# Optimization experiments

Hardware: AMD Instinct MI355X
Metric: run time of the kernel (lower is better)

The kernel has to match this reference:

```python
import jax, jax.numpy as jnp
import numpy as np
import math

C_S = 256
NUM_HEADS = 8
HEAD_DIM = 32
TOTAL = NUM_HEADS * HEAD_DIM
B, S, I = 1, 256, 256  # batch, msa sequences (column attn axis), residues
LN_EPS = 1e-5


def setup_inputs() -> dict:
    key = jax.random.key(0)
    ks = jax.random.split(key, 10)
    sc = 1.0 / math.sqrt(C_S)
    return {
        "msa": jax.random.normal(ks[0], (B, S, I, C_S), dtype=jnp.float32),
        "ln_gamma": jnp.ones((C_S,), dtype=jnp.float32),
        "ln_beta": jnp.zeros((C_S,), dtype=jnp.float32),
        "Wq": jax.random.normal(ks[1], (C_S, TOTAL), dtype=jnp.float32) * sc,
        "Wk": jax.random.normal(ks[2], (C_S, TOTAL), dtype=jnp.float32) * sc,
        "Wv": jax.random.normal(ks[3], (C_S, TOTAL), dtype=jnp.float32) * sc,
        "Wg": jax.random.normal(ks[4], (C_S, TOTAL), dtype=jnp.float32) * sc,
        "bg": jnp.zeros((TOTAL,), dtype=jnp.float32),
        "Wo": jax.random.normal(ks[5], (TOTAL, C_S), dtype=jnp.float32) * (1.0 / math.sqrt(TOTAL)),
        "bo": jnp.zeros((C_S,), dtype=jnp.float32),
    }


def reference(msa, ln_gamma, ln_beta, Wq, Wk, Wv, Wg, bg, Wo, bo):
    # LayerNorm over channel dim
    mu = jnp.mean(msa, axis=-1, keepdims=True)
    var = jnp.mean(jnp.square(msa - mu), axis=-1, keepdims=True)
    x = (msa - mu) * jax.lax.rsqrt(var + LN_EPS) * ln_gamma + ln_beta

    b, s, i, _ = x.shape
    hd = (NUM_HEADS, HEAD_DIM)
    Q = (x @ Wq).reshape(b, s, i, *hd)
    K = (x @ Wk).reshape(b, s, i, *hd)
    V = (x @ Wv).reshape(b, s, i, *hd)
    G = jax.nn.sigmoid((x @ Wg + bg).reshape(b, s, i, *hd))

    # column attention: contract over head_dim, attend over sequence axis s/t
    scores = jnp.einsum('bsihd,btihd->bihst', Q, K) / math.sqrt(HEAD_DIM)
    attn = jax.nn.softmax(scores, axis=-1)
    vals = jnp.einsum('bihst,btihd->bsihd', attn, V)

    vals = (G * vals).reshape(b, s, i, TOTAL)
    return vals @ Wo + bo
```

## Files before the change

kernel.cpp:

```cpp
#include <hip/hip_runtime.h>
#include <hip/hip_fp16.h>
#include <math.h>

#define C_S 256
#define NUM_HEADS 8
#define HEAD_DIM 32
#define TOTAL 256
#define S_DIM 256
#define I_DIM 256
#define NROWS (S_DIM * I_DIM)
#define LN_EPS 1e-5f

typedef _Float16 f16x8 __attribute__((ext_vector_type(8)));
typedef __attribute__((ext_vector_type(4))) float f32x4;

__device__ __forceinline__ ushort f2h(float x) {
  return __half_as_ushort(__float2half(x));
}
__device__ __forceinline__ float h2f(ushort u) {
  return __half2float(__ushort_as_half(u));
}
__device__ __forceinline__ void gl16(const void* g, void* l) {
  __builtin_amdgcn_global_load_lds(
      (const __attribute__((address_space(1))) unsigned*)g,
      (__attribute__((address_space(3))) unsigned*)l, 16, 0, 0);
}

__global__ __launch_bounds__(256) void prep_w_kernel(
    const float* __restrict__ Wq, const float* __restrict__ Wk,
    const float* __restrict__ Wv, const float* __restrict__ Wg,
    const float* __restrict__ Wo,
    ushort* __restrict__ Wch, ushort* __restrict__ Woh) {
  const int b = blockIdx.x;
  const int mat = b >> 8, n = b & 255;
  const int k = threadIdx.x;
  const float* W = (mat == 0) ? Wq : (mat == 1) ? Wk
                  : (mat == 2) ? Wv : (mat == 3) ? Wg : Wo;
  ushort h = f2h(W[(size_t)k * 256 + n]);
  if (mat < 4) Wch[((size_t)(mat * 256 + n)) * 256 + k] = h;
  else         Woh[(size_t)n * 256 + k] = h;
}

__global__ __launch_bounds__(256) void prep_x_kernel(
    const float* __restrict__ msa, const float* __restrict__ gamma,
    const float* __restrict__ beta, ushort* __restrict__ Xh) {
  const int row  = blockIdx.x * 4 + (threadIdx.x >> 6);
  const int lane = threadIdx.x & 63;
  float4 v = ((const float4*)(msa + (size_t)row * C_S))[lane];
  float sum = v.x + v.y + v.z + v.w;
  float sq  = v.x*v.x + v.y*v.y + v.z*v.z + v.w*v.w;
  #pragma unroll
  for (int off = 1; off < 64; off <<= 1) {
    sum += __shfl_xor(sum, off);
    sq  += __shfl_xor(sq, off);
  }
  float mu = sum * (1.0f / 256.0f);
  float rs = rsqrtf(sq * (1.0f / 256.0f) - mu * mu + LN_EPS);
  float4 gv = ((const float4*)gamma)[lane];
  float4 bv = ((const float4*)beta)[lane];
  ushort4 hh;
  hh.x = f2h((v.x - mu) * rs * gv.x + bv.x);
  hh.y = f2h((v.y - mu) * rs * gv.y + bv.y);
  hh.z = f2h((v.z - mu) * rs * gv.z + bv.z);
  hh.w = f2h((v.w - mu) * rs * gv.w + bv.w);
  *(ushort4*)(Xh + (size_t)row * 256 + lane * 4) = hh;
}

__global__ __launch_bounds__(256) void proj_kernel(
    const ushort* __restrict__ Xh, const ushort* __restrict__ Wch,
    const float* __restrict__ bg,
    ushort* __restrict__ Qh, ushort* __restrict__ Kh,
    ushort* __restrict__ Vh, __half* __restrict__ Gh) {
  __shared__ __align__(16) ushort At0[128 * 32];
  __shared__ __align__(16) ushort At1[128 * 32];
  __shared__ __align__(16) ushort Bt0[128 * 32];
  __shared__ __align__(16) ushort Bt1[128 * 32];

  const int bid = blockIdx.x;
  const int xcd = bid & 7;
  const int j   = bid >> 3;
  const int ntile = j & 7;
  const int rt    = (xcd << 6) + (j >> 3);
  const int n0 = ntile * 128;
  const int r0 = rt * 128;
  const int tid = threadIdx.x;
  const int wave = tid >> 6, lane = tid & 63;
  const int wm = wave >> 1, wn = wave & 1;
  const int lr = lane & 15, quad = lane >> 4;
  const int fsw = (quad ^ ((lr >> 1) & 3)) * 8;

  const int slot = wave * 64 + lane;
  const int row0 = slot >> 2;
  const int kc   = ((slot & 3) ^ ((row0 >> 1) & 3)) * 8;

  const ushort* pA = Xh + (size_t)(r0 + row0) * 256 + kc;
  const ushort* pB = Wch + (size_t)(n0 + row0) * 256 + kc;
  const int ld0 = wave * 512;
  const int ld1 = 2048 + wave * 512;

  f32x4 acc[4][4] = {};

  for (int kk = 0; kk < 4; ++kk) {
    __syncthreads();
    gl16(pA,             At0 + ld0); gl16(pA + 64 * 256,      At0 + ld1);
    gl16(pA + 32,        At1 + ld0); gl16(pA + 64 * 256 + 32, At1 + ld1);
    gl16(pB,             Bt0 + ld0); gl16(pB + 64 * 256,      Bt0 + ld1);
    gl16(pB + 32,        Bt1 + ld0); gl16(pB + 64 * 256 + 32, Bt1 + ld1);
    pA += 64; pB += 64;
    __syncthreads();

    f16x8 a0[4], a1[4], b0[4], b1[4];
    #pragma unroll
    for (int mt = 0; mt < 4; ++mt) {
      const int off = (wm * 64 + mt * 16 + lr) * 32 + fsw;
      a0[mt] = *(const f16x8*)&At0[off];
      a1[mt] = *(const f16x8*)&At1[off];
    }
    #pragma unroll
    for (int nt = 0; nt < 4; ++nt) {
      const int off = (wn * 64 + nt * 16 + lr) * 32 + fsw;
      b0[nt] = *(const f16x8*)&Bt0[off];
      b1[nt] = *(const f16x8*)&Bt1[off];
    }
    #pragma unroll
    for (int mt = 0; mt < 4; ++mt)
      #pragma unroll
      for (int nt = 0; nt < 4; ++nt) {
        acc[mt][nt] = __builtin_amdgcn_mfma_f32_16x16x32_f16(a0[mt], b0[nt], acc[mt][nt], 0, 0, 0);
        acc[mt][nt] = __builtin_amdgcn_mfma_f32_16x16x32_f16(a1[mt], b1[nt], acc[mt][nt], 0, 0, 0);
      }
  }

  const int region = ntile >> 1;
  const int nb = (ntile & 1) * 128;
  if (region == 3) {
    #pragma unroll
    for (int nt = 0; nt < 4; ++nt) {
      const int lcol = nb + wn * 64 + nt * 16 + lr;
      const float b = bg[lcol];
      #pragma unroll
      for (int mt = 0; mt < 4; ++mt)
        #pragma unroll
        for (int reg = 0; reg < 4; ++reg) {
          const int row = r0 + wm * 64 + mt * 16 + quad * 4 + reg;
          float v = acc[mt][nt][reg] + b;
          Gh[(size_t)row * TOTAL + lcol] = __float2half(1.0f / (1.0f + __expf(-v)));
        }
    }
  } else {
    ushort* P = (region == 0) ? Qh : (region == 1) ? Kh : Vh;
    const float scale = (region == 0) ? 0.25503534f : 1.0f;
    #pragma unroll
    for (int nt = 0; nt < 4; ++nt) {
      const int lcol = nb + wn * 64 + nt * 16 + lr;
      const int h = lcol >> 5, d = lcol & 31;
      #pragma unroll
      for (int mt = 0; mt < 4; ++mt)
        #pragma unroll
        for (int reg = 0; reg < 4; ++reg) {
          const int row = r0 + wm * 64 + mt * 16 + quad * 4 + reg;
          const int s = row >> 8, i = row & 255;
          P[(((size_t)(i * NUM_HEADS + h)) * S_DIM + s) * HEAD_DIM + d] =
              f2h(acc[mt][nt][reg] * scale);
        }
    }
  }
}

__global__ __launch_bounds__(256, 3) void attn_kernel(
    const ushort* Qh, const ushort* __restrict__ Kh,
    const ushort* __restrict__ Vh, const __half* __restrict__ Gh,
    ushort* Oh) {
  __shared__ __align__(16) ushort Ph[256][72];
  __shared__ __align__(16) ushort Vth[32][264];

  const int ih = blockIdx.x;
  const int i = ih >> 3, h = ih & 7;
  const int tid = threadIdx.x;
  const int wave = tid >> 6, lane = tid & 63;
  const int lr = lane & 15, quad = lane >> 4;
  const int s_base = wave * 64;
  const size_t hbase = (size_t)ih * (S_DIM * HEAD_DIM);

  {
    const uint4* vp = (const uint4*)(Vh + hbase + (size_t)tid * HEAD_DIM);
    #pragma unroll
    for (int jj = 0; jj < 4; ++jj) {
      uint4 w = vp[jj];
      unsigned ww[4] = {w.x, w.y, w.z, w.w};
      #pragma unroll
      for (int e = 0; e < 4; ++e) {
        Vth[jj * 8 + e * 2 + 0][tid] = (ushort)(ww[e] & 0xFFFFu);
        Vth[jj * 8 + e * 2 + 1][tid] = (ushort)(ww[e] >> 16);
      }
    }
  }
  __syncthreads();

  f16x8 qf[4];
  #pragma unroll
  for (int ns = 0; ns < 4; ++ns)
    qf[ns] = *(const f16x8*)(Qh + hbase +
                             (size_t)(s_base + ns * 16 + lr) * HEAD_DIM + quad * 8);

  f32x4 oacc[2][4] = {};
  float lpart[4] = {};

  #pragma unroll 1
  for (int c = 0; c < 4; ++c) {
    const int t0 = c * 64;
    f16x8 kf[4];
    #pragma unroll
    for (int mt = 0; mt < 4; ++mt)
      kf[mt] = *(const f16x8*)(Kh + hbase +
                               (size_t)(t0 + mt * 16 + lr) * HEAD_DIM + quad * 8);
    #pragma unroll
    for (int mt = 0; mt < 4; ++mt) {
      #pragma unroll
      for (int ns = 0; ns < 4; ++ns) {
        f32x4 sc = {};
        sc = __builtin_amdgcn_mfma_f32_16x16x32_f16(kf[mt], qf[ns], sc, 0, 0, 0);
        ushort u0 = f2h(exp2f(sc[0])), u1 = f2h(exp2f(sc[1]));
        ushort u2 = f2h(exp2f(sc[2])), u3 = f2h(exp2f(sc[3]));
        lpart[ns] += (h2f(u0) + h2f(u1)) + (h2f(u2) + h2f(u3));
        ushort4 pk = make_ushort4(u0, u1, u2, u3);
        *(ushort4*)&Ph[s_base + ns * 16 + lr][mt * 16 + quad * 4] = pk;
      }
    }
    #pragma unroll
    for (int ks = 0; ks < 2; ++ks) {
      const int tq = t0 + ks * 32 + quad * 8;
      f16x8 v0 = *(const f16x8*)&Vth[lr][tq];
      f16x8 v1 = *(const f16x8*)&Vth[16 + lr][tq];
      #pragma unroll
      for (int ns = 0; ns < 4; ++ns) {
        f16x8 pf = *(const f16x8*)&Ph[s_base + ns * 16 + lr][ks * 32 + quad * 8];
        oacc[0][ns] = __builtin_amdgcn_mfma_f32_16x16x32_f16(v0, pf, oacc[0][ns], 0, 0, 0);
        oacc[1][ns] = __builtin_amdgcn_mfma_f32_16x16x32_f16(v1, pf, oacc[1][ns], 0, 0, 0);
      }
    }
  }

  float invl[4];
  #pragma unroll
  for (int ns = 0; ns < 4; ++ns) {
    float v = lpart[ns];
    v += __shfl_xor(v, 16);
    v += __shfl_xor(v, 32);
    invl[ns] = 1.0f / v;
  }

  #pragma unroll
  for (int ns = 0; ns < 4; ++ns) {
    const int s = s_base + ns * 16 + lr;
    const __half* gp = Gh + ((size_t)(s * I_DIM + i)) * TOTAL + h * HEAD_DIM;
    #pragma unroll
    for (int md = 0; md < 2; ++md) {
      const int d0 = md * 16 + quad * 4;
      ushort4 ov;
      ov.x = f2h(__half2float(gp[d0 + 0]) * oacc[md][ns][0] * invl[ns]);
      ov.y = f2h(__half2float(gp[d0 + 1]) * oacc[md][ns][1] * invl[ns]);
      ov.z = f2h(__half2float(gp[d0 + 2]) * oacc[md][ns][2] * invl[ns]);
      ov.w = f2h(__half2float(gp[d0 + 3]) * oacc[md][ns][3] * invl[ns]);
      *(ushort4*)(Oh + hbase + (size_t)s * HEAD_DIM + d0) = ov;
    }
  }
}

__global__ __launch_bounds__(256) void out_kernel(
    const ushort* __restrict__ Oh, const ushort* __restrict__ Woh,
    const float* __restrict__ bo, float* __restrict__ out) {
  __shared__ __align__(16) ushort At0[128 * 32];
  __shared__ __align__(16) ushort At1[128 * 32];
  __shared__ __align__(16) ushort Bt0[128 * 32];
  __shared__ __align__(16) ushort Bt1[128 * 32];

  const int bid = blockIdx.x;
  const int xcd = bid & 7;
  const int j   = bid >> 3;
  const int ntile = j & 1;
  const int rg    = (xcd << 6) + (j >> 1);
  const int n0 = ntile * 128;
  const int s  = rg >> 1;
  const int i0 = (rg & 1) * 128;
  const int tid = threadIdx.x;
  const int wave = tid >> 6, lane = tid & 63;
  const int wm = wave >> 1, wn = wave & 1;
  const int lr = lane & 15, quad = lane >> 4;
  const int fsw = (quad ^ ((lr >> 1) & 3)) * 8;

  const int slot = wave * 64 + lane;
  const int row0 = slot >> 2;
  const int kc   = ((slot & 3) ^ ((row0 >> 1) & 3)) * 8;

  const ushort* pA = Oh + (size_t)(i0 + row0) * 65536 + (size_t)s * 32 + kc;
  const ushort* pB = Woh + (size_t)(n0 + row0) * 256 + kc;
  const int ld0 = wave * 512;
  const int ld1 = 2048 + wave * 512;

  f32x4 acc[4][4] = {};

  for (int kk = 0; kk < 4; ++kk) {
    __syncthreads();
    gl16(pA,               At0 + ld0); gl16(pA + (size_t)64 * 65536,        At0 + ld1);
    gl16(pA + 8192,        At1 + ld0); gl16(pA + (size_t)64 * 65536 + 8192, At1 + ld1);
    gl16(pB,               Bt0 + ld0); gl16(pB + 64 * 256,                  Bt0 + ld1);
    gl16(pB + 32,          Bt1 + ld0); gl16(pB + 64 * 256 + 32,             Bt1 + ld1);
    pA += 16384;
    pB += 64;
    __syncthreads();

    f16x8 a0[4], a1[4], b0[4], b1[4];
    #pragma unroll
    for (int mt = 0; mt < 4; ++mt) {
      const int off = (wm * 64 + mt * 16 + lr) * 32 + fsw;
      a0[mt] = *(const f16x8*)&At0[off];
      a1[mt] = *(const f16x8*)&At1[off];
    }
    #pragma unroll
    for (int nt = 0; nt < 4; ++nt) {
      const int off = (wn * 64 + nt * 16 + lr) * 32 + fsw;
      b0[nt] = *(const f16x8*)&Bt0[off];
      b1[nt] = *(const f16x8*)&Bt1[off];
    }
    #pragma unroll
    for (int mt = 0; mt < 4; ++mt)
      #pragma unroll
      for (int nt = 0; nt < 4; ++nt) {
        acc[mt][nt] = __builtin_amdgcn_mfma_f32_16x16x32_f16(a0[mt], b0[nt], acc[mt][nt], 0, 0, 0);
        acc[mt][nt] = __builtin_amdgcn_mfma_f32_16x16x32_f16(a1[mt], b1[nt], acc[mt][nt], 0, 0, 0);
      }
  }

  #pragma unroll
  for (int nt = 0; nt < 4; ++nt) {
    const int col = n0 + wn * 64 + nt * 16 + lr;
    const float b = bo[col];
    #pragma unroll
    for (int mt = 0; mt < 4; ++mt)
      #pragma unroll
      for (int reg = 0; reg < 4; ++reg) {
        const int mloc = wm * 64 + mt * 16 + quad * 4 + reg;
        out[((size_t)s * 256 + i0 + mloc) * C_S + col] = acc[mt][nt][reg] + b;
      }
  }
}

extern "C" void kernel_launch(void* const* d_in, const int* in_sizes, int n_in,
                              void* d_out, int out_size, void* d_ws, size_t ws_size,
                              hipStream_t stream) {
  const float* msa   = (const float*)d_in[0];
  const float* gamma = (const float*)d_in[1];
  const float* beta  = (const float*)d_in[2];
  const float* Wq    = (const float*)d_in[3];
  const float* Wk    = (const float*)d_in[4];
  const float* Wv    = (const float*)d_in[5];
  const float* Wg    = (const float*)d_in[6];
  const float* bg    = (const float*)d_in[7];
  const float* Wo    = (const float*)d_in[8];
  const float* bo    = (const float*)d_in[9];
  float* out = (float*)d_out;

  const size_t PLANE = (size_t)NROWS * TOTAL;
  ushort* Qh = (ushort*)d_ws;
  ushort* Kh = Qh + PLANE;
  ushort* Vh = Kh + PLANE;
  __half* Gh = (__half*)(Vh + PLANE);
  ushort* Wch = (ushort*)((ushort*)Gh + PLANE);
  ushort* Woh = Wch + 1024 * 256;
  ushort* Xh = (ushort*)d_out;

  prep_w_kernel<<<1280, 256, 0, stream>>>(Wq, Wk, Wv, Wg, Wo, Wch, Woh);
  prep_x_kernel<<<NROWS / 4, 256, 0, stream>>>(msa, gamma, beta, Xh);
  proj_kernel<<<4096, 256, 0, stream>>>(Xh, Wch, bg, Qh, Kh, Vh, Gh);
  attn_kernel<<<I_DIM * NUM_HEADS, 256, 0, stream>>>(Qh, Kh, Vh, Gh, Qh);
  out_kernel<<<1024, 256, 0, stream>>>(Qh, Woh, bo, out);
}
```

Measured before the change: 308.7 us.

## Fuse QKVG projection into column attention kernel, eliminating intermediate planes

Replaces the separate projection GEMM and attention kernels with one kernel per (residue, head) block. Each block computes its own Q, K, V and gate projections straight from the normalized input with MFMA, keeps K and V in LDS and the gate in registers, then runs attention. This removes the writes and reads of four large fp16 intermediate planes and one kernel launch. In exchange, the projection loads its X fragments directly from global memory with a strided pattern instead of staging tiles in LDS. Each X row is also re-read by all eight head blocks and twice within a block, and register pressure is high.

```diff
diff --git a/kernel.cpp b/kernel.cpp
--- a/kernel.cpp
+++ b/kernel.cpp
@@ -10,6 +10,7 @@
 #define I_DIM 256
 #define NROWS (S_DIM * I_DIM)
 #define LN_EPS 1e-5f
+#define QSCALE 0.25503534f
 
 typedef _Float16 f16x8 __attribute__((ext_vector_type(8)));
 typedef __attribute__((ext_vector_type(4))) float f32x4;
@@ -66,154 +67,122 @@
   *(ushort4*)(Xh + (size_t)row * 256 + lane * 4) = hh;
 }
 
-__global__ __launch_bounds__(256) void proj_kernel(
-    const ushort* __restrict__ Xh, const ushort* __restrict__ Wch,
+__global__ __launch_bounds__(256, 2) void fused_attn_kernel(
+    const ushort* __restrict__ Xh,
+    const ushort* __restrict__ Wch,
     const float* __restrict__ bg,
-    ushort* __restrict__ Qh, ushort* __restrict__ Kh,
-    ushort* __restrict__ Vh, __half* __restrict__ Gh) {
-  __shared__ __align__(16) ushort At0[128 * 32];
-  __shared__ __align__(16) ushort At1[128 * 32];
-  __shared__ __align__(16) ushort Bt0[128 * 32];
-  __shared__ __align__(16) ushort Bt1[128 * 32];
+    ushort* __restrict__ Oh) {
+  __shared__ __align__(16) ushort Kls[256][40];
+  __shared__ __align__(16) ushort Vth[32][264];
+  __shared__ __align__(16) ushort PQ[256][72];
 
   const int bid = blockIdx.x;
-  const int xcd = bid & 7;
-  const int j   = bid >> 3;
-  const int ntile = j & 7;
-  const int rt    = (xcd << 6) + (j >> 3);
-  const int n0 = ntile * 128;
-  const int r0 = rt * 128;
-  const int tid = threadIdx.x;
-  const int wave = tid >> 6, lane = tid & 63;
-  const int wm = wave >> 1, wn = wave & 1;
-  const int lr = lane & 15, quad = lane >> 4;
-  const int fsw = (quad ^ ((lr >> 1) & 3)) * 8;
-
-  const int slot = wave * 64 + lane;
-  const int row0 = slot >> 2;
-  const int kc   = ((slot & 3) ^ ((row0 >> 1) & 3)) * 8;
-
-  const ushort* pA = Xh + (size_t)(r0 + row0) * 256 + kc;
-  const ushort* pB = Wch + (size_t)(n0 + row0) * 256 + kc;
-  const int ld0 = wave * 512;
-  const int ld1 = 2048 + wave * 512;
-
-  f32x4 acc[4][4] = {};
-
-  for (int kk = 0; kk < 4; ++kk) {
-    __syncthreads();
-    gl16(pA,             At0 + ld0); gl16(pA + 64 * 256,      At0 + ld1);
-    gl16(pA + 32,        At1 + ld0); gl16(pA + 64 * 256 + 32, At1 + ld1);
-    gl16(pB,             Bt0 + ld0); gl16(pB + 64 * 256,      Bt0 + ld1);
-    gl16(pB + 32,        Bt1 + ld0); gl16(pB + 64 * 256 + 32, Bt1 + ld1);
-    pA += 64; pB += 64;
-    __syncthreads();
-
-    f16x8 a0[4], a1[4], b0[4], b1[4];
-    #pragma unroll
-    for (int mt = 0; mt < 4; ++mt) {
-      const int off = (wm * 64 + mt * 16 + lr) * 32 + fsw;
-      a0[mt] = *(const f16x8*)&At0[off];
-      a1[mt] = *(const f16x8*)&At1[off];
-    }
-    #pragma unroll
-    for (int nt = 0; nt < 4; ++nt) {
-      const int off = (wn * 64 + nt * 16 + lr) * 32 + fsw;
-      b0[nt] = *(const f16x8*)&Bt0[off];
-      b1[nt] = *(const f16x8*)&Bt1[off];
-    }
-    #pragma unroll
-    for (int mt = 0; mt < 4; ++mt)
-      #pragma unroll
-      for (int nt = 0; nt < 4; ++nt) {
-        acc[mt][nt] = __builtin_amdgcn_mfma_f32_16x16x32_f16(a0[mt], b0[nt], acc[mt][nt], 0, 0, 0);
-        acc[mt][nt] = __builtin_amdgcn_mfma_f32_16x16x32_f16(a1[mt], b1[nt], acc[mt][nt], 0, 0, 0);
-      }
-  }
-
-  const int region = ntile >> 1;
-  const int nb = (ntile & 1) * 128;
-  if (region == 3) {
-    #pragma unroll
-    for (int nt = 0; nt < 4; ++nt) {
-      const int lcol = nb + wn * 64 + nt * 16 + lr;
-      const float b = bg[lcol];
-      #pragma unroll
-      for (int mt = 0; mt < 4; ++mt)
-        #pragma unroll
-        for (int reg = 0; reg < 4; ++reg) {
-          const int row = r0 + wm * 64 + mt * 16 + quad * 4 + reg;
-          float v = acc[mt][nt][reg] + b;
-          Gh[(size_t)row * TOTAL + lcol] = __float2half(1.0f / (1.0f + __expf(-v)));
-        }
-    }
-  } else {
-    ushort* P = (region == 0) ? Qh : (region == 1) ? Kh : Vh;
-    const float scale = (region == 0) ? 0.25503534f : 1.0f;
-    #pragma unroll
-    for (int nt = 0; nt < 4; ++nt) {
-      const int lcol = nb + wn * 64 + nt * 16 + lr;
-      const int h = lcol >> 5, d = lcol & 31;
-      #pragma unroll
-      for (int mt = 0; mt < 4; ++mt)
-        #pragma unroll
-        for (int reg = 0; reg < 4; ++reg) {
-          const int row = r0 + wm * 64 + mt * 16 + quad * 4 + reg;
-          const int s = row >> 8, i = row & 255;
-          P[(((size_t)(i * NUM_HEADS + h)) * S_DIM + s) * HEAD_DIM + d] =
-              f2h(acc[mt][nt][reg] * scale);
-        }
-    }
-  }
-}
-
-__global__ __launch_bounds__(256, 3) void attn_kernel(
-    const ushort* Qh, const ushort* __restrict__ Kh,
-    const ushort* __restrict__ Vh, const __half* __restrict__ Gh,
-    ushort* Oh) {
-  __shared__ __align__(16) ushort Ph[256][72];
-  __shared__ __align__(16) ushort Vth[32][264];
-
-  const int ih = blockIdx.x;
-  const int i = ih >> 3, h = ih & 7;
+  const int xcd = bid & 7, j = bid >> 3;
+  const int h = j & 7;
+  const int i = (xcd << 5) + (j >> 3);
+  const int ih = i * NUM_HEADS + h;
   const int tid = threadIdx.x;
   const int wave = tid >> 6, lane = tid & 63;
   const int lr = lane & 15, quad = lane >> 4;
   const int s_base = wave * 64;
   const size_t hbase = (size_t)ih * (S_DIM * HEAD_DIM);
 
-  {
-    const uint4* vp = (const uint4*)(Vh + hbase + (size_t)tid * HEAD_DIM);
-    #pragma unroll
-    for (int jj = 0; jj < 4; ++jj) {
-      uint4 w = vp[jj];
-      unsigned ww[4] = {w.x, w.y, w.z, w.w};
-      #pragma unroll
-      for (int e = 0; e < 4; ++e) {
-        Vth[jj * 8 + e * 2 + 0][tid] = (ushort)(ww[e] & 0xFFFFu);
-        Vth[jj * 8 + e * 2 + 1][tid] = (ushort)(ww[e] >> 16);
-      }
-    }
-  }
+  const ushort* xr0 = Xh + ((size_t)(s_base + lr) * 256 + i) * 256 + quad * 8;
+  const ushort* wr0 = Wch + ((size_t)(h * 32 + lr)) * 256 + quad * 8;
+
+  f32x4 kacc[2][4] = {}, vacc[2][4] = {};
+  #pragma unroll
+  for (int kb = 0; kb < 8; ++kb) {
+    f16x8 xb[4];
+    #pragma unroll
+    for (int nt = 0; nt < 4; ++nt)
+      xb[nt] = *(const f16x8*)(xr0 + (size_t)nt * 16 * 65536 + kb * 32);
+    f16x8 wk[2], wv[2];
+    #pragma unroll
+    for (int mt = 0; mt < 2; ++mt) {
+      wk[mt] = *(const f16x8*)(wr0 + (size_t)1 * 65536 + mt * 4096 + kb * 32);
+      wv[mt] = *(const f16x8*)(wr0 + (size_t)2 * 65536 + mt * 4096 + kb * 32);
+    }
+    #pragma unroll
+    for (int mt = 0; mt < 2; ++mt)
+      #pragma unroll
+      for (int nt = 0; nt < 4; ++nt) {
+        kacc[mt][nt] = __builtin_amdgcn_mfma_f32_16x16x32_f16(wk[mt], xb[nt], kacc[mt][nt], 0, 0, 0);
+        vacc[mt][nt] = __builtin_amdgcn_mfma_f32_16x16x32_f16(wv[mt], xb[nt], vacc[mt][nt], 0, 0, 0);
+      }
+  }
+  #pragma unroll
+  for (int mt = 0; mt < 2; ++mt)
+    #pragma unroll
+    for (int nt = 0; nt < 4; ++nt) {
+      const int t = s_base + nt * 16 + lr;
+      ushort4 kp;
+      kp.x = f2h(kacc[mt][nt][0]); kp.y = f2h(kacc[mt][nt][1]);
+      kp.z = f2h(kacc[mt][nt][2]); kp.w = f2h(kacc[mt][nt][3]);
+      *(ushort4*)&Kls[t][mt * 16 + quad * 4] = kp;
+      #pragma unroll
+      for (int reg = 0; reg < 4; ++reg)
+        Vth[mt * 16 + quad * 4 + reg][t] = f2h(vacc[mt][nt][reg]);
+    }
+
+  f32x4 qacc[2][4] = {}, gacc[2][4] = {};
+  #pragma unroll
+  for (int kb = 0; kb < 8; ++kb) {
+    f16x8 xb[4];
+    #pragma unroll
+    for (int nt = 0; nt < 4; ++nt)
+      xb[nt] = *(const f16x8*)(xr0 + (size_t)nt * 16 * 65536 + kb * 32);
+    f16x8 wq[2], wg[2];
+    #pragma unroll
+    for (int mt = 0; mt < 2; ++mt) {
+      wq[mt] = *(const f16x8*)(wr0 + (size_t)0 * 65536 + mt * 4096 + kb * 32);
+      wg[mt] = *(const f16x8*)(wr0 + (size_t)3 * 65536 + mt * 4096 + kb * 32);
+    }
+    #pragma unroll
+    for (int mt = 0; mt < 2; ++mt)
+      #pragma unroll
+      for (int nt = 0; nt < 4; ++nt) {
+        qacc[mt][nt] = __builtin_amdgcn_mfma_f32_16x16x32_f16(wq[mt], xb[nt], qacc[mt][nt], 0, 0, 0);
+        gacc[mt][nt] = __builtin_amdgcn_mfma_f32_16x16x32_f16(wg[mt], xb[nt], gacc[mt][nt], 0, 0, 0);
+      }
+  }
+  #pragma unroll
+  for (int mt = 0; mt < 2; ++mt)
+    #pragma unroll
+    for (int nt = 0; nt < 4; ++nt) {
+      const int s = s_base + nt * 16 + lr;
+      ushort4 qp;
+      qp.x = f2h(qacc[mt][nt][0] * QSCALE); qp.y = f2h(qacc[mt][nt][1] * QSCALE);
+      qp.z = f2h(qacc[mt][nt][2] * QSCALE); qp.w = f2h(qacc[mt][nt][3] * QSCALE);
+      *(ushort4*)&PQ[s][mt * 16 + quad * 4] = qp;
+    }
+  f16x8 qf[4];
+  #pragma unroll
+  for (int ns = 0; ns < 4; ++ns)
+    qf[ns] = *(const f16x8*)&PQ[s_base + ns * 16 + lr][quad * 8];
+  f32x4 gv[2][4];
+  #pragma unroll
+  for (int mt = 0; mt < 2; ++mt) {
+    float4 bgv = *(const float4*)(bg + h * 32 + mt * 16 + quad * 4);
+    float bga[4] = {bgv.x, bgv.y, bgv.z, bgv.w};
+    #pragma unroll
+    for (int nt = 0; nt < 4; ++nt)
+      #pragma unroll
+      for (int reg = 0; reg < 4; ++reg)
+        gv[mt][nt][reg] = 1.0f / (1.0f + __expf(-(gacc[mt][nt][reg] + bga[reg])));
+  }
+
   __syncthreads();
-
-  f16x8 qf[4];
-  #pragma unroll
-  for (int ns = 0; ns < 4; ++ns)
-    qf[ns] = *(const f16x8*)(Qh + hbase +
-                             (size_t)(s_base + ns * 16 + lr) * HEAD_DIM + quad * 8);
 
   f32x4 oacc[2][4] = {};
   float lpart[4] = {};
-
   #pragma unroll 1
   for (int c = 0; c < 4; ++c) {
     const int t0 = c * 64;
     f16x8 kf[4];
     #pragma unroll
     for (int mt = 0; mt < 4; ++mt)
-      kf[mt] = *(const f16x8*)(Kh + hbase +
-                               (size_t)(t0 + mt * 16 + lr) * HEAD_DIM + quad * 8);
+      kf[mt] = *(const f16x8*)&Kls[t0 + mt * 16 + lr][quad * 8];
     #pragma unroll
     for (int mt = 0; mt < 4; ++mt) {
       #pragma unroll
@@ -224,7 +193,7 @@
         ushort u2 = f2h(exp2f(sc[2])), u3 = f2h(exp2f(sc[3]));
         lpart[ns] += (h2f(u0) + h2f(u1)) + (h2f(u2) + h2f(u3));
         ushort4 pk = make_ushort4(u0, u1, u2, u3);
-        *(ushort4*)&Ph[s_base + ns * 16 + lr][mt * 16 + quad * 4] = pk;
+        *(ushort4*)&PQ[s_base + ns * 16 + lr][mt * 16 + quad * 4] = pk;
       }
     }
     #pragma unroll
@@ -234,7 +203,7 @@
       f16x8 v1 = *(const f16x8*)&Vth[16 + lr][tq];
       #pragma unroll
       for (int ns = 0; ns < 4; ++ns) {
-        f16x8 pf = *(const f16x8*)&Ph[s_base + ns * 16 + lr][ks * 32 + quad * 8];
+        f16x8 pf = *(const f16x8*)&PQ[s_base + ns * 16 + lr][ks * 32 + quad * 8];
         oacc[0][ns] = __builtin_amdgcn_mfma_f32_16x16x32_f16(v0, pf, oacc[0][ns], 0, 0, 0);
         oacc[1][ns] = __builtin_amdgcn_mfma_f32_16x16x32_f16(v1, pf, oacc[1][ns], 0, 0, 0);
       }
@@ -253,15 +222,14 @@
   #pragma unroll
   for (int ns = 0; ns < 4; ++ns) {
     const int s = s_base + ns * 16 + lr;
-    const __half* gp = Gh + ((size_t)(s * I_DIM + i)) * TOTAL + h * HEAD_DIM;
     #pragma unroll
     for (int md = 0; md < 2; ++md) {
       const int d0 = md * 16 + quad * 4;
       ushort4 ov;
-      ov.x = f2h(__half2float(gp[d0 + 0]) * oacc[md][ns][0] * invl[ns]);
-      ov.y = f2h(__half2float(gp[d0 + 1]) * oacc[md][ns][1] * invl[ns]);
-      ov.z = f2h(__half2float(gp[d0 + 2]) * oacc[md][ns][2] * invl[ns]);
-      ov.w = f2h(__half2float(gp[d0 + 3]) * oacc[md][ns][3] * invl[ns]);
+      ov.x = f2h(gv[md][ns][0] * oacc[md][ns][0] * invl[ns]);
+      ov.y = f2h(gv[md][ns][1] * oacc[md][ns][1] * invl[ns]);
+      ov.z = f2h(gv[md][ns][2] * oacc[md][ns][2] * invl[ns]);
+      ov.w = f2h(gv[md][ns][3] * oacc[md][ns][3] * invl[ns]);
       *(ushort4*)(Oh + hbase + (size_t)s * HEAD_DIM + d0) = ov;
     }
   }
@@ -362,17 +330,13 @@
   float* out = (float*)d_out;
 
   const size_t PLANE = (size_t)NROWS * TOTAL;
-  ushort* Qh = (ushort*)d_ws;
-  ushort* Kh = Qh + PLANE;
-  ushort* Vh = Kh + PLANE;
-  __half* Gh = (__half*)(Vh + PLANE);
-  ushort* Wch = (ushort*)((ushort*)Gh + PLANE);
+  ushort* Oh  = (ushort*)d_ws;
+  ushort* Wch = Oh + PLANE;
   ushort* Woh = Wch + 1024 * 256;
   ushort* Xh = (ushort*)d_out;
 
   prep_w_kernel<<<1280, 256, 0, stream>>>(Wq, Wk, Wv, Wg, Wo, Wch, Woh);
   prep_x_kernel<<<NROWS / 4, 256, 0, stream>>>(msa, gamma, beta, Xh);
-  proj_kernel<<<4096, 256, 0, stream>>>(Xh, Wch, bg, Qh, Kh, Vh, Gh);
-  attn_kernel<<<I_DIM * NUM_HEADS, 256, 0, stream>>>(Qh, Kh, Vh, Gh, Qh);
-  out_kernel<<<1024, 256, 0, stream>>>(Qh, Woh, bo, out);
-}
+  fused_attn_kernel<<<I_DIM * NUM_HEADS, 256, 0, stream>>>(Xh, Wch, bg, Oh);
+  out_kernel<<<1024, 256, 0, stream>>>(Oh, Woh, bo, out);
+}
```

Result: faster. 284.2 us (-7.9%).
